# Kernel tuning notes

Measured on AMD Instinct MI355X. Metric: run time of the kernel, lower is better.

## Reference

```python
import jax, jax.numpy as jnp
import numpy as np

MAX_Z = 54  # atomic numbers up to iodine (53)
_mv = np.full(MAX_Z, 4.0, np.float32)
for z, v in {6: 4, 7: 3, 8: 2, 16: 6, 9: 1, 17: 1, 35: 1, 53: 1, 15: 5, 1: 1}.items():
    _mv[z] = v
_vdw = np.full(MAX_Z, 1.6, np.float32)  # default_radius = 1.6
for z, r in {1: 1.2, 6: 1.7, 7: 1.55, 8: 1.52, 9: 1.47, 15: 1.8, 16: 1.8, 17: 1.75, 35: 1.85, 53: 1.98}.items():
    _vdw[z] = r
_bl = np.full((MAX_Z, MAX_Z), 1.5, np.float32)  # default_length = 1.5
for (a, b), L in {(6, 6): 1.54, (6, 7): 1.47, (6, 8): 1.43, (6, 16): 1.82, (6, 9): 1.35, (6, 17): 1.77, (6, 1): 1.09, (7, 7): 1.45, (7, 8): 1.40, (7, 1): 1.01, (8, 8): 1.48, (8, 1): 0.96, (16, 16): 2.05, (15, 8): 1.63}.items():
    _bl[a, b] = L
    _bl[b, a] = L  # symmetric == tuple(sorted(...)) lookup
MAX_VAL = jnp.asarray(_mv)
VDW = jnp.asarray(_vdw)
BOND = jnp.asarray(_bl)
BIG = 1e9  # stands in for torch's float('inf') diagonal mask


def _forward(pos, edge_index, atom_types):
    N = pos.shape[0]
    row, col = edge_index[0], edge_index[1]
    # --- valence violations: scatter-add out-degree per atom ---
    bond_counts = jnp.zeros((N,), pos.dtype).at[row].add(1.0)
    violation = jnp.maximum(bond_counts - MAX_VAL[atom_types], 0.0)  # >0 iff counts > max_val
    loss = jnp.sum(violation ** 2)
    # Sequential valence push. Original loops atoms in ascending order and each atom's
    # neighbors in edge-list order; a stable sort of edges by row reproduces exactly that
    # visitation order, so a scan over sorted edges matches the sequential semantics
    # (pos_new[i] updates feed later direction computations).
    order = jnp.argsort(row)  # jnp.argsort is stable
    rs, cs = row[order], col[order]

    def step(p, rc):
        r, c = rc
        v = violation[r]
        d = p[r] - p[c]
        dist = jnp.linalg.norm(d) + 1e-8
        return p.at[r].add(jnp.where(v > 0, d / dist * v * 1e-3, 0.0)), None

    pos_new, _ = jax.lax.scan(step, pos, (rs, cs))
    # --- bond-length correction (gather per edge, scatter back per atom) ---
    bond_vec = pos_new[row] - pos_new[col]                        # [E,3]
    cur_len = jnp.linalg.norm(bond_vec, axis=-1, keepdims=True)   # [E,1]
    tgt_len = BOND[atom_types[row], atom_types[col]][:, None]     # [E,1]
    loss = loss + jnp.mean(jnp.abs(cur_len - tgt_len) ** 2)
    ratio = jnp.clip(tgt_len / (cur_len + 1e-8), 0.98, 1.02)
    adj = (bond_vec * ratio - bond_vec) * 0.01
    pos_new = pos_new + jnp.zeros_like(pos).at[row].add(adj * 0.5).at[col].add(-adj * 0.5)
    # --- steric clash repulsion over all atom pairs (cdist) ---
    sq = jnp.sum(pos_new ** 2, axis=-1)
    d2 = sq[:, None] + sq[None, :] - 2.0 * (pos_new @ pos_new.T)  # [N,N]
    eye = jnp.eye(N, dtype=bool)
    dist = jnp.sqrt(jnp.maximum(jnp.where(eye, 1.0, d2), 1e-20))
    dist = jnp.where(eye, BIG, dist)  # diagonal masked to +inf in the original
    rad = VDW[atom_types]
    min_d = (rad[:, None] + rad[None, :]) * 0.8
    loss = loss + jnp.sum(jax.nn.relu(min_d - dist) ** 2) / 2.0
    # original loops unordered clash pairs i<j updating i and j symmetrically; the full
    # symmetric double sum below is mathematically identical and avoids an [N,N,3] tensor:
    mask = (dist < min_d) & (dist > 1e-8)
    coeff = jnp.where(mask, (min_d - dist) * 0.005 * 0.5 / dist, 0.0)  # [N,N]
    steric = coeff.sum(axis=1)[:, None] * pos_new - coeff @ pos_new    # sum_j c_ij (p_i - p_j)
    return pos_new + steric, loss * 0.1


def setup_inputs() -> dict:
    key = jax.random.key(0)
    k1, k2, k3, k4 = jax.random.split(key, 4)
    N, E = 8192, 32768
    pos = jax.random.normal(k1, (N, 3), jnp.float32) * 6.0  # coords in an ~Angstrom-scale blob
    elements = jnp.array([1, 6, 7, 8, 9, 15, 16, 17], jnp.int32)  # H C N O F P S Cl
    atom_types = elements[jax.random.randint(k2, (N,), 0, 8)]
    edge_index = jnp.stack([jax.random.randint(k3, (E,), 0, N),
                            jax.random.randint(k4, (E,), 0, N)]).astype(jnp.int32)
    return {"pos": pos, "edge_index": edge_index, "atom_types": atom_types}


def reference(pos, edge_index, atom_types):
    return _forward(pos, edge_index, atom_types)
```

## Files before the change

### kernel.cpp

```cpp
#include <hip/hip_runtime.h>
#include <math.h>

#define NA 8192
#define NE 32768
#define NT 256
#define NCH 32
#define CHUNK 128
#define IBLK 512
#define NIB (NA / IBLK)
#define NPAD 4096
#define NSLICE NCH

#define NBIN 256
#define XMIN (-32.0f)
#define BW 0.25f
#define INVBW 4.0f
#define MDMAX 3.168f
#define SKIPM 3.40f
#define BSHIFT 13

#define WS_DEG      0
#define WS_BINCNT   (WS_DEG + NA)
#define WS_MEMSET_N (WS_BINCNT + NBIN)
#define WS_LOSS     WS_MEMSET_N
#define WS_DD       (WS_LOSS + 4)
#define WS_BINSTART (WS_DD + 3*NA)
#define WS_BINOF    (WS_BINSTART + NBIN)
#define WS_PD       ((WS_BINOF + NA + 3) & ~3)
#define WS_SPD      (WS_PD + 4*NA)
#define WS_SORIG    (WS_SPD + 4*(NA+NPAD))
#define WS_PART     ((WS_SORIG + NA + 3) & ~3)

__device__ __forceinline__ float maxval_of(int z) {
    switch (z) {
        case 1: return 1.f; case 6: return 4.f; case 7: return 3.f; case 8: return 2.f;
        case 9: return 1.f; case 15: return 5.f; case 16: return 6.f; case 17: return 1.f;
        case 35: return 1.f; case 53: return 1.f; default: return 4.f;
    }
}
__device__ __forceinline__ float vdw_of(int z) {
    switch (z) {
        case 1: return 1.2f; case 6: return 1.7f; case 7: return 1.55f; case 8: return 1.52f;
        case 9: return 1.47f; case 15: return 1.8f; case 16: return 1.8f; case 17: return 1.75f;
        case 35: return 1.85f; case 53: return 1.98f; default: return 1.6f;
    }
}
__device__ __forceinline__ float bond_of(int a, int b) {
    int lo = a < b ? a : b, hi = a < b ? b : a;
    switch (lo * 64 + hi) {
        case 6*64+6:   return 1.54f;
        case 6*64+7:   return 1.47f;
        case 6*64+8:   return 1.43f;
        case 6*64+16:  return 1.82f;
        case 6*64+9:   return 1.35f;
        case 6*64+17:  return 1.77f;
        case 1*64+6:   return 1.09f;
        case 7*64+7:   return 1.45f;
        case 7*64+8:   return 1.40f;
        case 1*64+7:   return 1.01f;
        case 8*64+8:   return 1.48f;
        case 1*64+8:   return 0.96f;
        case 16*64+16: return 2.05f;
        case 8*64+15:  return 1.63f;
        default:       return 1.5f;
    }
}
__device__ __forceinline__ float viol_of(int d, int z) {
    return fmaxf((float)d - maxval_of(z), 0.f);
}
__device__ __forceinline__ int bin_of_x(float x) {
    int b = (int)floorf((x - XMIN) * INVBW);
    return min(max(b, 0), NBIN - 1);
}

__device__ __forceinline__ float wave_reduce_sum(float x) {
    #pragma unroll
    for (int off = 32; off > 0; off >>= 1) x += __shfl_down(x, off);
    return x;
}

__global__ void k_deg(const int* __restrict__ row, int* __restrict__ deg,
                      float* __restrict__ zbase ) {
    int e = blockIdx.x * NT + threadIdx.x;
    if (e < 3 * NA + 4) zbase[e] = 0.f;
    if (e < NE) atomicAdd(&deg[row[e]], 1);
}

__global__ void k_edge(const int* __restrict__ row, const int* __restrict__ col,
                       const int* __restrict__ types, const int* __restrict__ deg,
                       const float* __restrict__ pos, float* __restrict__ dD,
                       float* __restrict__ lossAcc) {
    int e = blockIdx.x * NT + threadIdx.x;
    float l1 = 0.f, l0 = 0.f;
    if (e < NE) {
        int r = row[e], c = col[e];
        float bx = pos[3*r]   - pos[3*c];
        float by = pos[3*r+1] - pos[3*c+1];
        float bz = pos[3*r+2] - pos[3*c+2];
        float cur = sqrtf(bx*bx + by*by + bz*bz);
        float tgt = bond_of(types[r], types[c]);
        float diff = cur - tgt;
        l1 = diff * diff;
        float ratio = tgt / (cur + 1e-8f);
        ratio = fminf(fmaxf(ratio, 0.98f), 1.02f);
        float s = (ratio - 1.f) * 0.01f * 0.5f;
        float v = viol_of(deg[r], types[r]);
        float sc = (v > 0.f) ? (v * 1e-3f / (cur + 1e-8f)) : 0.f;
        float rs = s + sc;
        atomicAdd(&dD[3*r],   bx * rs);
        atomicAdd(&dD[3*r+1], by * rs);
        atomicAdd(&dD[3*r+2], bz * rs);
        atomicAdd(&dD[3*c],   -bx * s);
        atomicAdd(&dD[3*c+1], -by * s);
        atomicAdd(&dD[3*c+2], -bz * s);
    }
    if (e < NA) {
        float v = viol_of(deg[e], types[e]);
        l0 = v * v;
    }
    float p1 = wave_reduce_sum(l1);
    float p0 = wave_reduce_sum(l0);
    if ((threadIdx.x & 63) == 0) {
        if (p1 != 0.f) atomicAdd(&lossAcc[1], p1);
        if (p0 != 0.f) atomicAdd(&lossAcc[0], p0);
    }
}

__global__ void k_pack(const float* __restrict__ pos, const float* __restrict__ dD,
                       const int* __restrict__ types, float4* __restrict__ pd,
                       float4* __restrict__ spd, int* __restrict__ binOf,
                       int* __restrict__ binCnt) {
    int a = blockIdx.x * NT + threadIdx.x;
    float4 v = make_float4(pos[3*a]   + dD[3*a],
                           pos[3*a+1] + dD[3*a+1],
                           pos[3*a+2] + dD[3*a+2],
                           vdw_of(types[a]) * 0.8f);
    pd[a] = v;
    int b = bin_of_x(v.x);
    int rank = atomicAdd(&binCnt[b], 1);
    binOf[a] = b | (rank << 8);
    if (a < NPAD) spd[NA + a] = make_float4(1e9f, 1e9f, 1e9f, 0.f);
}

__global__ void k_scatter(const float4* __restrict__ pd, const int* __restrict__ binOf,
                          const int* __restrict__ binCnt, int* __restrict__ binStartG,
                          float4* __restrict__ spd, int* __restrict__ sorig) {
    __shared__ int buf[NBIN];
    const int t = threadIdx.x;
    buf[t] = binCnt[t];
    __syncthreads();
    int own = buf[t];
    for (int off = 1; off < NBIN; off <<= 1) {
        int v = (t >= off) ? buf[t - off] : 0;
        __syncthreads();
        buf[t] += v;
        __syncthreads();
    }
    __shared__ int sStart[NBIN];
    sStart[t] = buf[t] - own;
    if (blockIdx.x == 0) binStartG[t] = buf[t] - own;
    __syncthreads();
    int a = blockIdx.x * NT + t;
    int v = binOf[a];
    int dst = sStart[v & 255] + (v >> 8);
    spd[dst] = pd[a];
    sorig[dst] = a;
}

__device__ __forceinline__ void steric_pair(const float4 p, const float4 q,
                                            float& cs, float& sx, float& sy, float& sz,
                                            float& ll) {
    float dx = p.x - q.x, dy = p.y - q.y, dz = p.z - q.z;
    float d2 = fmaf(dx, dx, fmaf(dy, dy, dz * dz));
    float md = p.w + q.w;
    float rinv = rsqrtf(fmaxf(d2, 1e-12f));
    float dist = d2 * rinv;
    float t1 = md - dist;
    bool ok = (t1 > 0.f) && (d2 > 1e-12f);
    float t1c = ok ? t1 : 0.f;
    ll = fmaf(t1c, t1c, ll);
    float co = t1c * rinv;
    cs += co;
    sx = fmaf(co, q.x, sx);
    sy = fmaf(co, q.y, sy);
    sz = fmaf(co, q.z, sz);
}

__global__ void __launch_bounds__(NT)
k_steric(const float4* __restrict__ spd, const int* __restrict__ binStart,
         float4* __restrict__ partial, float* __restrict__ lossAcc) {
    __shared__ float4 sm[CHUNK];
    const int t = threadIdx.x;
    const int b = blockIdx.x;
    const int ib = b >> 5;
    const int c  = b & 31;
    const int i0 = ib * IBLK + t;
    const int i1 = i0 + NT;
    float xlo = spd[ib * IBLK].x;
    float xhi = spd[ib * IBLK + IBLK - 1].x;
    int bs = bin_of_x(xlo) - BSHIFT; bs = bs < 0 ? 0 : bs;
    const int jbase = binStart[bs] + c * CHUNK;
    if (spd[jbase].x > xhi + SKIPM || spd[jbase + CHUNK - 1].x < xlo - SKIPM) {
        float4 z = make_float4(0.f, 0.f, 0.f, 0.f);
        partial[c * NA + i0] = z;
        partial[c * NA + i1] = z;
        return;
    }
    if (t < CHUNK) sm[t] = spd[jbase + t];
    float4 p0 = spd[i0];
    float4 p1 = spd[i1];
    __syncthreads();
    float cs0 = 0.f, sx0 = 0.f, sy0 = 0.f, sz0 = 0.f, ll0 = 0.f;
    float cs1 = 0.f, sx1 = 0.f, sy1 = 0.f, sz1 = 0.f, ll1 = 0.f;
    #pragma unroll 8
    for (int jj = 0; jj < CHUNK; jj++) {
        float4 q = sm[jj];
        steric_pair(p0, q, cs0, sx0, sy0, sz0, ll0);
        steric_pair(p1, q, cs1, sx1, sy1, sz1, ll1);
    }
    partial[c * NA + i0] = make_float4(cs0, sx0, sy0, sz0);
    partial[c * NA + i1] = make_float4(cs1, sx1, sy1, sz1);
    float part = wave_reduce_sum(ll0 + ll1);
    if ((t & 63) == 0 && part != 0.f) atomicAdd(&lossAcc[2], part);
}

__global__ void k_reduce(const float4* __restrict__ spd, const int* __restrict__ sorig,
                         const float4* __restrict__ partial,
                         const float* __restrict__ lossAcc, float* __restrict__ out) {
    int s = blockIdx.x * NT + threadIdx.x;
    float cs = 0.f, sx = 0.f, sy = 0.f, sz = 0.f;
    #pragma unroll 8
    for (int y = 0; y < NSLICE; y++) {
        float4 u = partial[y * NA + s];
        cs += u.x; sx += u.y; sy += u.z; sz += u.w;
    }
    float4 p = spd[s];
    float c = 1.f + cs * 0.0025f;
    int orig = sorig[s];
    out[3*orig]   = p.x * c - sx * 0.0025f;
    out[3*orig+1] = p.y * c - sy * 0.0025f;
    out[3*orig+2] = p.z * c - sz * 0.0025f;
    if (s == 0) {
        float loss = lossAcc[0] + lossAcc[1] * (1.f / NE) + lossAcc[2] * 0.5f;
        out[3*NA] = loss * 0.1f;
    }
}

extern "C" void kernel_launch(void* const* d_in, const int* in_sizes, int n_in,
                              void* d_out, int out_size, void* d_ws, size_t ws_size,
                              hipStream_t stream) {
    (void)in_sizes; (void)n_in; (void)out_size; (void)ws_size;
    const float* pos   = (const float*)d_in[0];
    const int*   eidx  = (const int*)d_in[1];
    const int*   types = (const int*)d_in[2];
    const int* row = eidx;
    const int* col = eidx + NE;

    int*   ws_i = (int*)d_ws;
    float* ws_f = (float*)d_ws;
    int*    deg      = ws_i + WS_DEG;
    int*    binCnt   = ws_i + WS_BINCNT;
    float*  lossAcc  = ws_f + WS_LOSS;
    float*  dD       = ws_f + WS_DD;
    int*    binStart = ws_i + WS_BINSTART;
    int*    binOf    = ws_i + WS_BINOF;
    float4* pd       = (float4*)(ws_f + WS_PD);
    float4* spd      = (float4*)(ws_f + WS_SPD);
    int*    sorig    = ws_i + WS_SORIG;
    float4* partial  = (float4*)(ws_f + WS_PART);
    float*  out      = (float*)d_out;

    hipMemsetAsync(d_ws, 0, (size_t)WS_MEMSET_N * 4, stream);
    k_deg    <<<NE/NT, NT, 0, stream>>>(row, deg, ws_f + WS_LOSS);
    k_edge   <<<NE/NT, NT, 0, stream>>>(row, col, types, deg, pos, dD, lossAcc);
    k_pack   <<<NA/NT, NT, 0, stream>>>(pos, dD, types, pd, spd, binOf, binCnt);
    k_scatter<<<NA/NT, NT, 0, stream>>>(pd, binOf, binCnt, binStart, spd, sorig);
    k_steric <<<NIB*NCH, NT, 0, stream>>>(spd, binStart, partial, lossAcc);
    k_reduce <<<NA/NT, NT, 0, stream>>>(spd, sorig, partial, lossAcc, out);
}
```

Before: 127.8 us.

## Bin atoms by original x in k_deg, drop k_pack, widen steric window

Atoms are now binned by their original x coordinate inside k_deg, which lets the separate k_pack kernel and the pd buffer go away. k_scatter builds the final float4 records directly and also computes, by binary search, the bin holding each i-block's first sorted atom. Because sorted positions now include the bond-correction shift and are only approximately ordered, the steric j-window grows from 32 to 33 chunks and the skip margin widens. This removes one launch and one round trip through global memory, at the cost of slightly more steric blocks and some reliance on bond displacements staying small.

After: 129.2 us. About the same (+1.1%).

```diff
diff --git a/kernel.cpp b/kernel.cpp
--- a/kernel.cpp
+++ b/kernel.cpp
@@ -4,19 +4,18 @@
 #define NA 8192
 #define NE 32768
 #define NT 256
-#define NCH 32
+#define NCH 33
 #define CHUNK 128
 #define IBLK 512
 #define NIB (NA / IBLK)
-#define NPAD 4096
+#define NPAD 4352
 #define NSLICE NCH
 
 #define NBIN 256
 #define XMIN (-32.0f)
 #define BW 0.25f
 #define INVBW 4.0f
-#define MDMAX 3.168f
-#define SKIPM 3.40f
+#define SKIPM 3.50f
 #define BSHIFT 13
 
 #define WS_DEG      0
@@ -25,9 +24,9 @@
 #define WS_LOSS     WS_MEMSET_N
 #define WS_DD       (WS_LOSS + 4)
 #define WS_BINSTART (WS_DD + 3*NA)
-#define WS_BINOF    (WS_BINSTART + NBIN)
-#define WS_PD       ((WS_BINOF + NA + 3) & ~3)
-#define WS_SPD      (WS_PD + 4*NA)
+#define WS_IBBIN    (WS_BINSTART + NBIN)
+#define WS_BINOF    (WS_IBBIN + NIB)
+#define WS_SPD      ((WS_BINOF + NA + 3) & ~3)
 #define WS_SORIG    (WS_SPD + 4*(NA+NPAD))
 #define WS_PART     ((WS_SORIG + NA + 3) & ~3)
 
@@ -79,10 +78,18 @@
     return x;
 }
 
-__global__ void k_deg(const int* __restrict__ row, int* __restrict__ deg,
+__global__ void k_deg(const int* __restrict__ row, const float* __restrict__ pos,
+                      int* __restrict__ deg, int* __restrict__ binCnt,
+                      int* __restrict__ binOf, float4* __restrict__ spd,
                       float* __restrict__ zbase ) {
     int e = blockIdx.x * NT + threadIdx.x;
     if (e < 3 * NA + 4) zbase[e] = 0.f;
+    if (e < NPAD) spd[NA + e] = make_float4(1e9f, 1e9f, 1e9f, 0.f);
+    if (e < NA) {
+        int b = bin_of_x(pos[3*e]);
+        int rank = atomicAdd(&binCnt[b], 1);
+        binOf[e] = b | (rank << 8);
+    }
     if (e < NE) atomicAdd(&deg[row[e]], 1);
 }
 
@@ -126,26 +133,13 @@
     }
 }
 
-__global__ void k_pack(const float* __restrict__ pos, const float* __restrict__ dD,
-                       const int* __restrict__ types, float4* __restrict__ pd,
-                       float4* __restrict__ spd, int* __restrict__ binOf,
-                       int* __restrict__ binCnt) {
-    int a = blockIdx.x * NT + threadIdx.x;
-    float4 v = make_float4(pos[3*a]   + dD[3*a],
-                           pos[3*a+1] + dD[3*a+1],
-                           pos[3*a+2] + dD[3*a+2],
-                           vdw_of(types[a]) * 0.8f);
-    pd[a] = v;
-    int b = bin_of_x(v.x);
-    int rank = atomicAdd(&binCnt[b], 1);
-    binOf[a] = b | (rank << 8);
-    if (a < NPAD) spd[NA + a] = make_float4(1e9f, 1e9f, 1e9f, 0.f);
-}
-
-__global__ void k_scatter(const float4* __restrict__ pd, const int* __restrict__ binOf,
+__global__ void k_scatter(const float* __restrict__ pos, const float* __restrict__ dD,
+                          const int* __restrict__ types, const int* __restrict__ binOf,
                           const int* __restrict__ binCnt, int* __restrict__ binStartG,
+                          int* __restrict__ ibBinG,
                           float4* __restrict__ spd, int* __restrict__ sorig) {
     __shared__ int buf[NBIN];
+    __shared__ int sStart[NBIN];
     const int t = threadIdx.x;
     buf[t] = binCnt[t];
     __syncthreads();
@@ -156,14 +150,23 @@
         buf[t] += v;
         __syncthreads();
     }
-    __shared__ int sStart[NBIN];
     sStart[t] = buf[t] - own;
-    if (blockIdx.x == 0) binStartG[t] = buf[t] - own;
+    if (blockIdx.x == 0) binStartG[t] = sStart[t];
     __syncthreads();
+    if (blockIdx.x == 0 && t < NIB) {
+        int S = t * IBLK;
+        int lo = 0, hi = NBIN;
+        while (lo < hi) { int mid = (lo + hi) >> 1;
+                          if (sStart[mid] <= S) lo = mid + 1; else hi = mid; }
+        ibBinG[t] = lo - 1;
+    }
     int a = blockIdx.x * NT + t;
     int v = binOf[a];
     int dst = sStart[v & 255] + (v >> 8);
-    spd[dst] = pd[a];
+    spd[dst] = make_float4(pos[3*a]   + dD[3*a],
+                           pos[3*a+1] + dD[3*a+1],
+                           pos[3*a+2] + dD[3*a+2],
+                           vdw_of(types[a]) * 0.8f);
     sorig[dst] = a;
 }
 
@@ -188,17 +191,18 @@
 
 __global__ void __launch_bounds__(NT)
 k_steric(const float4* __restrict__ spd, const int* __restrict__ binStart,
+         const int* __restrict__ ibBin,
          float4* __restrict__ partial, float* __restrict__ lossAcc) {
     __shared__ float4 sm[CHUNK];
     const int t = threadIdx.x;
     const int b = blockIdx.x;
-    const int ib = b >> 5;
-    const int c  = b & 31;
+    const int ib = b / NCH;
+    const int c  = b % NCH;
     const int i0 = ib * IBLK + t;
     const int i1 = i0 + NT;
     float xlo = spd[ib * IBLK].x;
     float xhi = spd[ib * IBLK + IBLK - 1].x;
-    int bs = bin_of_x(xlo) - BSHIFT; bs = bs < 0 ? 0 : bs;
+    int bs = ibBin[ib] - BSHIFT; bs = bs < 0 ? 0 : bs;
     const int jbase = binStart[bs] + c * CHUNK;
     if (spd[jbase].x > xhi + SKIPM || spd[jbase + CHUNK - 1].x < xlo - SKIPM) {
         float4 z = make_float4(0.f, 0.f, 0.f, 0.f);
@@ -229,7 +233,7 @@
                          const float* __restrict__ lossAcc, float* __restrict__ out) {
     int s = blockIdx.x * NT + threadIdx.x;
     float cs = 0.f, sx = 0.f, sy = 0.f, sz = 0.f;
-    #pragma unroll 8
+    #pragma unroll 3
     for (int y = 0; y < NSLICE; y++) {
         float4 u = partial[y * NA + s];
         cs += u.x; sx += u.y; sy += u.z; sz += u.w;
@@ -263,18 +267,19 @@
     float*  lossAcc  = ws_f + WS_LOSS;
     float*  dD       = ws_f + WS_DD;
     int*    binStart = ws_i + WS_BINSTART;
+    int*    ibBin    = ws_i + WS_IBBIN;
     int*    binOf    = ws_i + WS_BINOF;
-    float4* pd       = (float4*)(ws_f + WS_PD);
     float4* spd      = (float4*)(ws_f + WS_SPD);
     int*    sorig    = ws_i + WS_SORIG;
     float4* partial  = (float4*)(ws_f + WS_PART);
     float*  out      = (float*)d_out;
 
     hipMemsetAsync(d_ws, 0, (size_t)WS_MEMSET_N * 4, stream);
-    k_deg    <<<NE/NT, NT, 0, stream>>>(row, deg, ws_f + WS_LOSS);
+    k_deg    <<<NE/NT, NT, 0, stream>>>(row, pos, deg, binCnt, binOf, spd,
+                                        ws_f + WS_LOSS);
     k_edge   <<<NE/NT, NT, 0, stream>>>(row, col, types, deg, pos, dD, lossAcc);
-    k_pack   <<<NA/NT, NT, 0, stream>>>(pos, dD, types, pd, spd, binOf, binCnt);
-    k_scatter<<<NA/NT, NT, 0, stream>>>(pd, binOf, binCnt, binStart, spd, sorig);
-    k_steric <<<NIB*NCH, NT, 0, stream>>>(spd, binStart, partial, lossAcc);
+    k_scatter<<<NA/NT, NT, 0, stream>>>(pos, dD, types, binOf, binCnt,
+                                        binStart, ibBin, spd, sorig);
+    k_steric <<<NIB*NCH, NT, 0, stream>>>(spd, binStart, ibBin, partial, lossAcc);
     k_reduce <<<NA/NT, NT, 0, stream>>>(spd, sorig, partial, lossAcc, out);
 }
```
